# Kernel optimization log

Hardware: AMD Instinct MI355X
Metric: run time of the kernel (lower is better)

Reference implementation:

```python
import jax, jax.numpy as jnp
import numpy as np
import math

NUM_HEADS = 16
EPS = 1e-5

# Single-step spikingjelly LIFNode(tau=2.0, v_threshold=1.0, v_reset=0.0):
#   v = (x - 0)/tau = x/2 ; spike = heaviside(v - 1) = (x >= 2)
@jax.custom_vjp
def lif(x):
    return (x >= 2.0).astype(x.dtype)

def _lif_fwd(x):
    return (x >= 2.0).astype(x.dtype), x

def _lif_bwd(x, g):
    # sigmoid surrogate (alpha=4) on v - v_th, chained through dv/dx = 1/tau = 0.5
    s = jax.nn.sigmoid(4.0 * (0.5 * x - 1.0))
    return (g * (4.0 * s * (1.0 - s)) * 0.5,)

lif.defvjp(_lif_fwd, _lif_bwd)

def layernorm(x, gamma, beta):
    mu = jnp.mean(x, axis=-1, keepdims=True)
    var = jnp.var(x, axis=-1, keepdims=True)
    return (x - mu) * jax.lax.rsqrt(var + EPS) * gamma + beta

def mish(x):
    return x * jnp.tanh(jax.nn.softplus(x))

def setup_inputs() -> dict:
    key = jax.random.key(0)
    ks = jax.random.split(key, 8)
    B, Sq, Skv, dQ, dK, dV = 8, 1024, 1024, 1024, 1024, 1024
    def xavier_normal(k, shape):
        std = math.sqrt(2.0 / (shape[0] + shape[1]))
        return jax.random.normal(k, shape, jnp.float32) * std
    return {
        "Q": jax.random.normal(ks[0], (B, Sq, dQ), jnp.float32) * 2.0,
        "K": jax.random.normal(ks[1], (B, Skv, dK), jnp.float32) * 2.0,
        "adj_mask": (jax.random.uniform(ks[2], (B, 1, Sq, Skv)) < 0.7).astype(jnp.float32),
        "Wq": xavier_normal(ks[3], (dV, dQ)), "bq": jnp.zeros((dV,), jnp.float32),
        "Wk": xavier_normal(ks[4], (dV, dK)), "bk": jnp.zeros((dV,), jnp.float32),
        "Wv": xavier_normal(ks[5], (dV, dK)), "bv": jnp.zeros((dV,), jnp.float32),
        "Wo": xavier_normal(ks[6], (dV, dV)), "bo": jnp.zeros((dV,), jnp.float32),
        "g_q": jnp.ones((dV,), jnp.float32), "be_q": jnp.zeros((dV,), jnp.float32),
        "g_k": jnp.ones((dV,), jnp.float32), "be_k": jnp.zeros((dV,), jnp.float32),
    }

def reference(Q, K, adj_mask, Wq, bq, Wk, bk, Wv, bv, Wo, bo, g_q, be_q, g_k, be_k):
    B, Sq, _ = Q.shape
    Skv = K.shape[1]
    dV = Wq.shape[0]
    hd = dV // NUM_HEADS
    # LIF-gated projections (eval mode: dropout off)
    q = lif(layernorm(lif(Q) @ Wq.T + bq, g_q, be_q))          # [B,Sq,dV] binary
    v = lif(K) @ Wv.T + bv                                      # fc_v(k_lif(K))
    k = lif(layernorm(lif(K) @ Wk.T + bk, g_k, be_k))          # K(k_norm(fc_k(v_lif(K))))
    q = q.reshape(B, Sq, NUM_HEADS, hd).transpose(0, 2, 1, 3)  # [B,H,Sq,hd]
    k = k.reshape(B, Skv, NUM_HEADS, hd).transpose(0, 2, 1, 3)
    v = v.reshape(B, Skv, NUM_HEADS, hd).transpose(0, 2, 1, 3)
    scores = jnp.einsum('bhqd,bhkd->bhqk', q, k) / math.sqrt(hd)
    scores = scores * adj_mask                                  # multiplicative mask
    w = jax.nn.softmax(scores, axis=-1)
    out = jnp.einsum('bhqk,bhkd->bhqd', w, v)
    out = out.transpose(0, 2, 1, 3).reshape(B, Sq, dV)
    o = out @ Wo.T + bo
    return out + mish(o)
```

## Files before the change

kernel.cpp:

```cpp
#include <hip/hip_runtime.h>
#include <hip/hip_bf16.h>

typedef __attribute__((ext_vector_type(4))) float fx4;
typedef __attribute__((ext_vector_type(8))) short bv8;
typedef unsigned int u32;
typedef unsigned short u16;
typedef __hip_bfloat16 bf16;

#define DEVI static __device__ __forceinline__

static constexpr int NBATCH = 8;
static constexpr int SEQ = 1024;
static constexpr int DM  = 1024;
static constexpr int NH  = 16;
static constexpr int MROWS = NBATCH * SEQ;
static constexpr size_t SZ = (size_t)MROWS * DM;

DEVI void gl16(const void* g, void* l) {
  __builtin_amdgcn_global_load_lds((const __attribute__((address_space(1))) void*)g,
                                   (__attribute__((address_space(3))) void*)l, 16, 0, 0);
}
DEVI fx4 mfma_bf16(bv8 a, bv8 b, fx4 c) {
  return __builtin_amdgcn_mfma_f32_16x16x32_bf16(a, b, c, 0, 0, 0);
}

__global__ __launch_bounds__(256) void prep_weights(
    const float* __restrict__ wq, const float* __restrict__ wk,
    const float* __restrict__ wv, const float* __restrict__ wo,
    bf16* __restrict__ qh, bf16* __restrict__ qm, bf16* __restrict__ ql,
    bf16* __restrict__ kh, bf16* __restrict__ km, bf16* __restrict__ kl,
    bf16* __restrict__ vb, bf16* __restrict__ ob)
{
  int i = (blockIdx.x * 256 + threadIdx.x) * 4;
  int w = blockIdx.y;
  const float* src = (w == 0) ? wq : (w == 1) ? wk : (w == 2) ? wv : wo;
  fx4 v = *(const fx4*)&src[i];
  if (w < 2) {
    bf16* hi = (w == 0) ? qh : kh;
    bf16* mi = (w == 0) ? qm : km;
    bf16* lo = (w == 0) ? ql : kl;
#pragma unroll
    for (int j = 0; j < 4; j++) {
      float x = v[j];
      bf16 h = __float2bfloat16(x);
      float r1 = x - __bfloat162float(h);
      bf16 m = __float2bfloat16(r1);
      float r2 = r1 - __bfloat162float(m);
      hi[i + j] = h;
      mi[i + j] = m;
      lo[i + j] = __float2bfloat16(r2);
    }
  } else {
    bf16* dst = (w == 2) ? vb : ob;
#pragma unroll
    for (int j = 0; j < 4; j++) dst[i + j] = __float2bfloat16(v[j]);
  }
}

__global__ __launch_bounds__(256) void spike_kernel(const float* __restrict__ x, u16* __restrict__ o)
{
  size_t i = ((size_t)blockIdx.x * 256 + threadIdx.x) * 4;
  fx4 v = *(const fx4*)&x[i];
  u32 a = (v[0] >= 2.f ? 0x3F80u : 0u) | ((v[1] >= 2.f ? 0x3F80u : 0u) << 16);
  u32 b = (v[2] >= 2.f ? 0x3F80u : 0u) | ((v[3] >= 2.f ? 0x3F80u : 0u) << 16);
  u32* p = (u32*)(o + i);
  p[0] = a; p[1] = b;
}

__global__ __launch_bounds__(256) void maskpack_kernel(const float* __restrict__ m, u32* __restrict__ w)
{
  size_t gid = (size_t)blockIdx.x * 256 + threadIdx.x;
  unsigned long long bal = __ballot(m[gid] != 0.0f);
  int lane = threadIdx.x & 63;
  if (lane == 0) w[gid >> 5] = (u32)bal;
  else if (lane == 32) w[gid >> 5] = (u32)(bal >> 32);
}

template<int NB, int EPI>
__global__ __launch_bounds__(256) void gemm_bt(
    const bf16* __restrict__ A, const bf16* __restrict__ B0, const bf16* __restrict__ B1,
    const bf16* __restrict__ B2,
    const float* __restrict__ bias, const float* __restrict__ addsrc,
    float* __restrict__ Cf, bf16* __restrict__ Cb, int K, int N)
{
  __shared__ __attribute__((aligned(16))) bf16 sA[128 * 64];
  __shared__ __attribute__((aligned(16))) bf16 sB[NB * 128 * 64];
  const bf16* Bp[3] = {B0, B1, B2};
  const int tid = threadIdx.x;
  const int lane = tid & 63, wave = tid >> 6;
  const int wr = wave >> 1, wc = wave & 1;
  const int l15 = lane & 15, l4 = lane >> 4;
  const int rowBase = blockIdx.x * 128;
  const int colBase = blockIdx.y * 128;

  fx4 acc[4][4];
#pragma unroll
  for (int m = 0; m < 4; m++) {
#pragma unroll
    for (int n = 0; n < 4; n++) acc[m][n] = fx4{0.f, 0.f, 0.f, 0.f};
  }

  for (int kt = 0; kt < K; kt += 64) {
#pragma unroll
    for (int i = 0; i < 4; i++) {
      int c = i * 256 + tid;
      int r = c >> 3, cb = (c & 7) * 8;
      gl16(A + (size_t)(rowBase + r) * K + kt + cb, &sA[c * 8]);
    }
#pragma unroll
    for (int b = 0; b < NB; b++) {
#pragma unroll
      for (int i = 0; i < 4; i++) {
        int c = i * 256 + tid;
        int r = c >> 3, cb = (c & 7) * 8;
        gl16(Bp[b] + (size_t)(colBase + r) * K + kt + cb, &sB[b * 128 * 64 + c * 8]);
      }
    }
    __syncthreads();
#pragma unroll
    for (int kk = 0; kk < 2; kk++) {
      bv8 af[4];
#pragma unroll
      for (int m = 0; m < 4; m++)
        af[m] = *(const bv8*)&sA[(wr * 64 + m * 16 + l15) * 64 + kk * 32 + l4 * 8];
#pragma unroll
      for (int b = 0; b < NB; b++) {
#pragma unroll
        for (int n = 0; n < 4; n++) {
          bv8 bfr = *(const bv8*)&sB[b * 128 * 64 + (wc * 64 + n * 16 + l15) * 64 + kk * 32 + l4 * 8];
#pragma unroll
          for (int m = 0; m < 4; m++) acc[m][n] = mfma_bf16(af[m], bfr, acc[m][n]);
        }
      }
    }
    __syncthreads();
  }
#pragma unroll
  for (int n = 0; n < 4; n++) {
    int col = colBase + wc * 64 + n * 16 + l15;
    float bvv = bias[col];
#pragma unroll
    for (int m = 0; m < 4; m++) {
      int row0 = rowBase + wr * 64 + m * 16 + l4 * 4;
#pragma unroll
      for (int r = 0; r < 4; r++) {
        size_t idx = (size_t)(row0 + r) * N + col;
        float val = acc[m][n][r] + bvv;
        if (EPI == 0) {
          Cf[idx] = val;
        } else if (EPI == 1) {
          Cb[idx] = __float2bfloat16(val);
        } else {
          float sp = log1pf(__expf(val));
          Cf[idx] = addsrc[idx] + val * tanhf(sp);
        }
      }
    }
  }
}

__global__ __launch_bounds__(256) void lnlif_kernel(
    const float* __restrict__ x, const float* __restrict__ g, const float* __restrict__ be,
    u16* __restrict__ out)
{
  __shared__ float red[4];
  const int row = blockIdx.x;
  const int tid = threadIdx.x;
  fx4 v = *(const fx4*)&x[(size_t)row * DM + tid * 4];
  float s = v[0] + v[1] + v[2] + v[3];
#pragma unroll
  for (int off = 1; off < 64; off <<= 1) s += __shfl_xor(s, off, 64);
  if ((tid & 63) == 0) red[tid >> 6] = s;
  __syncthreads();
  float mean = (red[0] + red[1] + red[2] + red[3]) * (1.0f / 1024.0f);
  __syncthreads();
  float d0 = v[0] - mean, d1 = v[1] - mean, d2 = v[2] - mean, d3 = v[3] - mean;
  float ss = d0 * d0 + d1 * d1 + d2 * d2 + d3 * d3;
#pragma unroll
  for (int off = 1; off < 64; off <<= 1) ss += __shfl_xor(ss, off, 64);
  if ((tid & 63) == 0) red[tid >> 6] = ss;
  __syncthreads();
  float var = (red[0] + red[1] + red[2] + red[3]) * (1.0f / 1024.0f);
  float rstd = rsqrtf(var + 1e-5f);
  const int c = tid * 4;
  fx4 gg = *(const fx4*)&g[c];
  fx4 bb = *(const fx4*)&be[c];
  float y0 = d0 * rstd * gg[0] + bb[0];
  float y1 = d1 * rstd * gg[1] + bb[1];
  float y2 = d2 * rstd * gg[2] + bb[2];
  float y3 = d3 * rstd * gg[3] + bb[3];
  u32 a = (y0 >= 2.f ? 0x3F80u : 0u) | ((y1 >= 2.f ? 0x3F80u : 0u) << 16);
  u32 b = (y2 >= 2.f ? 0x3F80u : 0u) | ((y3 >= 2.f ? 0x3F80u : 0u) << 16);
  u32* p = (u32*)(out + (size_t)row * DM + c);
  p[0] = a; p[1] = b;
}

__global__ __launch_bounds__(256) void transpose_v(const bf16* __restrict__ v, bf16* __restrict__ vt)
{
  __shared__ bf16 t[64][72];
  const int tc = blockIdx.x, tr = blockIdx.y, b = blockIdx.z;
  const int tid = threadIdx.x;
  const size_t base = (size_t)b * SEQ * DM;
#pragma unroll
  for (int i = 0; i < 2; i++) {
    int c = i * 256 + tid;
    int r = c >> 3, cg = (c & 7) * 8;
    bv8 val = *(const bv8*)&v[base + (size_t)(tr * 64 + r) * DM + tc * 64 + cg];
#pragma unroll
    for (int j = 0; j < 8; j++) t[r][cg + j] = ((const bf16*)&val)[j];
  }
  __syncthreads();
#pragma unroll
  for (int i = 0; i < 2; i++) {
    int c = i * 256 + tid;
    int r = c >> 3, cg = (c & 7) * 8;
    bf16 tmp[8];
#pragma unroll
    for (int j = 0; j < 8; j++) tmp[j] = t[cg + j][r];
    *(bv8*)&vt[base + (size_t)(tc * 64 + r) * SEQ + tr * 64 + cg] = *(const bv8*)tmp;
  }
}

__global__ __launch_bounds__(256) void attn_kernel(
    const bf16* __restrict__ qb, const bf16* __restrict__ kb, const bf16* __restrict__ vt,
    const u32* __restrict__ mw, float* __restrict__ of, bf16* __restrict__ ob)
{
  __shared__ __attribute__((aligned(16))) bf16 sQ[64 * 64];
  __shared__ __attribute__((aligned(16))) bf16 sK[64 * 64];
  __shared__ __attribute__((aligned(16))) bf16 sV[64 * 64];
  __shared__ __attribute__((aligned(16))) bf16 sP[4][16 * 64];
  __shared__ u32 sM[128];
  const int qt = blockIdx.x, h = blockIdx.y, b = blockIdx.z;
  const int tid = threadIdx.x, lane = tid & 63, wave = tid >> 6;
  const int l15 = lane & 15, l4 = lane >> 4;
  const size_t qrow0 = (size_t)b * SEQ + qt * 64;

#pragma unroll
  for (int i = 0; i < 2; i++) {
    int c = i * 256 + tid;
    int r = c >> 3, cg = (c & 7) * 8;
    gl16(qb + (qrow0 + r) * DM + h * 64 + cg, &sQ[c * 8]);
  }
  __syncthreads();
  bv8 af[2];
  af[0] = *(const bv8*)&sQ[(wave * 16 + l15) * 64 + l4 * 8];
  af[1] = *(const bv8*)&sQ[(wave * 16 + l15) * 64 + 32 + l4 * 8];

  fx4 acc_o[4];
#pragma unroll
  for (int n = 0; n < 4; n++) acc_o[n] = fx4{0.f, 0.f, 0.f, 0.f};
  float rowsum[4] = {0.f, 0.f, 0.f, 0.f};

  for (int kvb = 0; kvb < SEQ; kvb += 64) {
#pragma unroll
    for (int i = 0; i < 2; i++) {
      int c = i * 256 + tid;
      int r = c >> 3, cg = (c & 7) * 8;
      gl16(kb + ((size_t)b * SEQ + kvb + r) * DM + h * 64 + cg, &sK[c * 8]);
      gl16(vt + (size_t)b * SEQ * DM + (size_t)(h * 64 + r) * SEQ + kvb + cg, &sV[c * 8]);
    }
    if (tid < 128) sM[tid] = mw[(qrow0 + (tid >> 1)) * 32 + (kvb >> 5) + (tid & 1)];
    __syncthreads();

    fx4 accs[4];
#pragma unroll
    for (int n = 0; n < 4; n++) accs[n] = fx4{0.f, 0.f, 0.f, 0.f};
#pragma unroll
    for (int kk = 0; kk < 2; kk++) {
#pragma unroll
      for (int n = 0; n < 4; n++) {
        bv8 bfk = *(const bv8*)&sK[(n * 16 + l15) * 64 + kk * 32 + l4 * 8];
        accs[n] = mfma_bf16(af[kk], bfk, accs[n]);
      }
    }
    float prow[4] = {0.f, 0.f, 0.f, 0.f};
#pragma unroll
    for (int n = 0; n < 4; n++) {
#pragma unroll
      for (int r = 0; r < 4; r++) {
        u32 wd = sM[((wave << 4) + (l4 << 2) + r) * 2 + (n >> 1)];
        float sc = accs[n][r] * 0.125f;
        float p = ((wd >> ((n & 1) * 16 + l15)) & 1u) ? __expf(sc) : 1.0f;
        prow[r] += p;
        sP[wave][((l4 << 2) + r) * 64 + n * 16 + l15] = __float2bfloat16(p);
      }
    }
#pragma unroll
    for (int r = 0; r < 4; r++) {
      float t2 = prow[r];
      t2 += __shfl_xor(t2, 1, 64);
      t2 += __shfl_xor(t2, 2, 64);
      t2 += __shfl_xor(t2, 4, 64);
      t2 += __shfl_xor(t2, 8, 64);
      rowsum[r] += t2;
    }
    __syncthreads();
#pragma unroll
    for (int kk = 0; kk < 2; kk++) {
      bv8 pa = *(const bv8*)&sP[wave][l15 * 64 + kk * 32 + l4 * 8];
#pragma unroll
      for (int n = 0; n < 4; n++) {
        bv8 bvv = *(const bv8*)&sV[(n * 16 + l15) * 64 + kk * 32 + l4 * 8];
        acc_o[n] = mfma_bf16(pa, bvv, acc_o[n]);
      }
    }
    __syncthreads();
  }
#pragma unroll
  for (int r = 0; r < 4; r++) {
    float inv = 1.0f / rowsum[r];
    size_t row = qrow0 + wave * 16 + (l4 << 2) + r;
#pragma unroll
    for (int n = 0; n < 4; n++) {
      size_t idx = row * DM + h * 64 + n * 16 + l15;
      float val = acc_o[n][r] * inv;
      of[idx] = val;
      ob[idx] = __float2bfloat16(val);
    }
  }
}

extern "C" void kernel_launch(void* const* d_in, const int* in_sizes, int n_in,
                              void* d_out, int out_size, void* d_ws, size_t ws_size,
                              hipStream_t stream) {
  (void)in_sizes; (void)n_in; (void)out_size; (void)ws_size;
  const float* Q    = (const float*)d_in[0];
  const float* Kin  = (const float*)d_in[1];
  const float* mask = (const float*)d_in[2];
  const float* Wq   = (const float*)d_in[3];
  const float* bq   = (const float*)d_in[4];
  const float* Wk   = (const float*)d_in[5];
  const float* bk   = (const float*)d_in[6];
  const float* Wv   = (const float*)d_in[7];
  const float* bv   = (const float*)d_in[8];
  const float* Wo   = (const float*)d_in[9];
  const float* bo   = (const float*)d_in[10];
  const float* g_q  = (const float*)d_in[11];
  const float* be_q = (const float*)d_in[12];
  const float* g_k  = (const float*)d_in[13];
  const float* be_k = (const float*)d_in[14];
  float* out = (float*)d_out;

  char* w = (char*)d_ws;
  size_t off = 0;
  auto alloc = [&](size_t bytes) -> char* {
    char* p = w + off;
    off += (bytes + 255) & ~(size_t)255;
    return p;
  };
  bf16* q_spike = (bf16*)alloc(SZ * 2);
  bf16* k_spike = (bf16*)alloc(SZ * 2);
  float* xq     = (float*)alloc(SZ * 4);
  float* xk     = (float*)alloc(SZ * 4);
  bf16* vb_     = (bf16*)alloc(SZ * 2);
  bf16* vtb     = (bf16*)alloc(SZ * 2);
  u32* mwords   = (u32*)alloc(SZ / 32 * 4);
  bf16* whq = (bf16*)alloc((size_t)DM * DM * 2);
  bf16* wmq = (bf16*)alloc((size_t)DM * DM * 2);
  bf16* wlq = (bf16*)alloc((size_t)DM * DM * 2);
  bf16* whk = (bf16*)alloc((size_t)DM * DM * 2);
  bf16* wmk = (bf16*)alloc((size_t)DM * DM * 2);
  bf16* wlk = (bf16*)alloc((size_t)DM * DM * 2);
  bf16* wvb = (bf16*)alloc((size_t)DM * DM * 2);
  bf16* wob = (bf16*)alloc((size_t)DM * DM * 2);
  bf16* qbn = q_spike;
  bf16* kbn = k_spike;
  float* attn_out = xq;
  bf16* attn_outb = (bf16*)xk;

  prep_weights<<<dim3(DM * DM / 1024, 4), 256, 0, stream>>>(Wq, Wk, Wv, Wo,
                                                            whq, wmq, wlq, whk, wmk, wlk, wvb, wob);
  spike_kernel<<<SZ / 1024, 256, 0, stream>>>(Q, (u16*)q_spike);
  spike_kernel<<<SZ / 1024, 256, 0, stream>>>(Kin, (u16*)k_spike);
  maskpack_kernel<<<SZ / 256, 256, 0, stream>>>(mask, mwords);

  gemm_bt<3, 0><<<dim3(64, 8), 256, 0, stream>>>(q_spike, whq, wmq, wlq, bq, nullptr, xq, nullptr, DM, DM);
  gemm_bt<3, 0><<<dim3(64, 8), 256, 0, stream>>>(k_spike, whk, wmk, wlk, bk, nullptr, xk, nullptr, DM, DM);
  gemm_bt<1, 1><<<dim3(64, 8), 256, 0, stream>>>(k_spike, wvb, nullptr, nullptr, bv, nullptr, nullptr, vb_, DM, DM);

  lnlif_kernel<<<MROWS, 256, 0, stream>>>(xq, g_q, be_q, (u16*)qbn);
  lnlif_kernel<<<MROWS, 256, 0, stream>>>(xk, g_k, be_k, (u16*)kbn);
  transpose_v<<<dim3(16, 16, NBATCH), 256, 0, stream>>>(vb_, vtb);

  attn_kernel<<<dim3(16, NH, NBATCH), 256, 0, stream>>>(qbn, kbn, vtb, mwords, attn_out, attn_outb);

  gemm_bt<1, 2><<<dim3(64, 8), 256, 0, stream>>>(attn_outb, wob, nullptr, nullptr, bo, attn_out, out, nullptr, DM, DM);
}
```

Baseline: 523.8 us.

## Double-buffer K/V tiles in attention with swizzled LDS and transposed mask words

The attention kernel now double-buffers the K, V and mask tiles so the next tile's global-to-LDS loads are issued while the current tile is computed, using one barrier per iteration instead of three. LDS layouts for K, V and P are XOR-swizzled to avoid bank conflicts. The packed mask is stored transposed so each block loads its mask words with vector loads. The row-sum shuffle reduction moves out of the loop, Q fragments are read directly from global memory, and exp becomes exp2 with a prescaled constant. It also adds s_setprio hints around the MFMA blocks. The cost is twice the LDS for K/V, and the single barrier relies on the per-wave sP buffer being safely reused across iterations.

```diff
diff --git a/kernel.cpp b/kernel.cpp
--- a/kernel.cpp
+++ b/kernel.cpp
@@ -72,8 +72,12 @@
   size_t gid = (size_t)blockIdx.x * 256 + threadIdx.x;
   unsigned long long bal = __ballot(m[gid] != 0.0f);
   int lane = threadIdx.x & 63;
-  if (lane == 0) w[gid >> 5] = (u32)bal;
-  else if (lane == 32) w[gid >> 5] = (u32)(bal >> 32);
+  u32 skv = (u32)(gid & 1023);
+  u32 sq  = (u32)((gid >> 10) & 1023);
+  u32 b   = (u32)(gid >> 20);
+  size_t oidx = (size_t)b * 32768 + (skv >> 5) * 1024 + sq;
+  if (lane == 0) w[oidx] = (u32)bal;
+  else if (lane == 32) w[oidx] = (u32)(bal >> 32);
 }
 
 template<int NB, int EPI>
@@ -223,92 +227,115 @@
 
 __global__ __launch_bounds__(256) void attn_kernel(
     const bf16* __restrict__ qb, const bf16* __restrict__ kb, const bf16* __restrict__ vt,
-    const u32* __restrict__ mw, float* __restrict__ of, bf16* __restrict__ ob)
-{
-  __shared__ __attribute__((aligned(16))) bf16 sQ[64 * 64];
-  __shared__ __attribute__((aligned(16))) bf16 sK[64 * 64];
-  __shared__ __attribute__((aligned(16))) bf16 sV[64 * 64];
+    const u32* __restrict__ mwT, float* __restrict__ of, bf16* __restrict__ ob)
+{
+  __shared__ __attribute__((aligned(16))) bf16 sK[2][64 * 64];
+  __shared__ __attribute__((aligned(16))) bf16 sV[2][64 * 64];
   __shared__ __attribute__((aligned(16))) bf16 sP[4][16 * 64];
-  __shared__ u32 sM[128];
+  __shared__ __attribute__((aligned(16))) u32 sM[2][128];
   const int qt = blockIdx.x, h = blockIdx.y, b = blockIdx.z;
   const int tid = threadIdx.x, lane = tid & 63, wave = tid >> 6;
   const int l15 = lane & 15, l4 = lane >> 4;
   const size_t qrow0 = (size_t)b * SEQ + qt * 64;
-
-#pragma unroll
-  for (int i = 0; i < 2; i++) {
-    int c = i * 256 + tid;
-    int r = c >> 3, cg = (c & 7) * 8;
-    gl16(qb + (qrow0 + r) * DM + h * 64 + cg, &sQ[c * 8]);
-  }
-  __syncthreads();
-  bv8 af[2];
-  af[0] = *(const bv8*)&sQ[(wave * 16 + l15) * 64 + l4 * 8];
-  af[1] = *(const bv8*)&sQ[(wave * 16 + l15) * 64 + 32 + l4 * 8];
-
-  fx4 acc_o[4];
-#pragma unroll
-  for (int n = 0; n < 4; n++) acc_o[n] = fx4{0.f, 0.f, 0.f, 0.f};
-  float rowsum[4] = {0.f, 0.f, 0.f, 0.f};
-
-  for (int kvb = 0; kvb < SEQ; kvb += 64) {
+  const bf16* kB = kb + (size_t)b * SEQ * DM + h * 64;
+  const bf16* vB = vt + (size_t)b * SEQ * DM + (size_t)(h * 64) * SEQ;
+  const u32*  mB = mwT + (size_t)b * 32768 + qt * 64;
+
+  auto STAGE = [&](int t, int buf) {
+    const int kvb = t * 64;
 #pragma unroll
     for (int i = 0; i < 2; i++) {
       int c = i * 256 + tid;
-      int r = c >> 3, cg = (c & 7) * 8;
-      gl16(kb + ((size_t)b * SEQ + kvb + r) * DM + h * 64 + cg, &sK[c * 8]);
-      gl16(vt + (size_t)b * SEQ * DM + (size_t)(h * 64 + r) * SEQ + kvb + cg, &sV[c * 8]);
-    }
-    if (tid < 128) sM[tid] = mw[(qrow0 + (tid >> 1)) * 32 + (kvb >> 5) + (tid & 1)];
-    __syncthreads();
+      int row = c >> 3;
+      int sb = ((c & 7) * 16) ^ ((row & 7) << 4);
+      gl16(kB + (size_t)(kvb + row) * DM + (sb >> 1), &sK[buf][c * 8]);
+      gl16(vB + (size_t)row * SEQ + kvb + (sb >> 1), &sV[buf][c * 8]);
+    }
+    if (tid < 32) {
+      int w = tid >> 4, rg = (tid & 15) * 4;
+      uint4 mv = *(const uint4*)&mB[(size_t)(t * 2 + w) * 1024 + rg];
+      *(uint4*)&sM[buf][w * 64 + rg] = mv;
+    }
+  };
+
+  bv8 af[2];
+#pragma unroll
+  for (int kk = 0; kk < 2; kk++)
+    af[kk] = *(const bv8*)&qb[(qrow0 + wave * 16 + l15) * DM + h * 64 + kk * 32 + l4 * 8];
+
+  fx4 acc_o[4];
+#pragma unroll
+  for (int n = 0; n < 4; n++) acc_o[n] = fx4{0.f, 0.f, 0.f, 0.f};
+  float psum[4] = {0.f, 0.f, 0.f, 0.f};
+
+  char* sPw = (char*)sP[wave];
+  STAGE(0, 0);
+
+  for (int t = 0; t < 16; t++) {
+    const int cur = t & 1;
+    asm volatile("s_waitcnt vmcnt(0) lgkmcnt(0)" ::: "memory");
+    __builtin_amdgcn_s_barrier();
+    if (t < 15) STAGE(t + 1, cur ^ 1);
+
+    const char* sKc = (const char*)sK[cur];
+    const char* sVc = (const char*)sV[cur];
 
     fx4 accs[4];
 #pragma unroll
     for (int n = 0; n < 4; n++) accs[n] = fx4{0.f, 0.f, 0.f, 0.f};
+    __builtin_amdgcn_s_setprio(1);
 #pragma unroll
     for (int kk = 0; kk < 2; kk++) {
 #pragma unroll
       for (int n = 0; n < 4; n++) {
-        bv8 bfk = *(const bv8*)&sK[(n * 16 + l15) * 64 + kk * 32 + l4 * 8];
-        accs[n] = mfma_bf16(af[kk], bfk, accs[n]);
-      }
-    }
-    float prow[4] = {0.f, 0.f, 0.f, 0.f};
+        int row = n * 16 + l15;
+        bv8 bk8 = *(const bv8*)(sKc + row * 128 + ((kk * 64 + l4 * 16) ^ ((row & 7) << 4)));
+        accs[n] = mfma_bf16(af[kk], bk8, accs[n]);
+      }
+    }
+    __builtin_amdgcn_s_setprio(0);
+
+    uint4 m0 = *(const uint4*)&sM[cur][wave * 16 + l4 * 4];
+    uint4 m1 = *(const uint4*)&sM[cur][64 + wave * 16 + l4 * 4];
+    u32 sh0[4] = {m0.x >> l15, m0.y >> l15, m0.z >> l15, m0.w >> l15};
+    u32 sh1[4] = {m1.x >> l15, m1.y >> l15, m1.z >> l15, m1.w >> l15};
+
 #pragma unroll
     for (int n = 0; n < 4; n++) {
 #pragma unroll
       for (int r = 0; r < 4; r++) {
-        u32 wd = sM[((wave << 4) + (l4 << 2) + r) * 2 + (n >> 1)];
-        float sc = accs[n][r] * 0.125f;
-        float p = ((wd >> ((n & 1) * 16 + l15)) & 1u) ? __expf(sc) : 1.0f;
-        prow[r] += p;
-        sP[wave][((l4 << 2) + r) * 64 + n * 16 + l15] = __float2bfloat16(p);
-      }
-    }
-#pragma unroll
-    for (int r = 0; r < 4; r++) {
-      float t2 = prow[r];
-      t2 += __shfl_xor(t2, 1, 64);
-      t2 += __shfl_xor(t2, 2, 64);
-      t2 += __shfl_xor(t2, 4, 64);
-      t2 += __shfl_xor(t2, 8, 64);
-      rowsum[r] += t2;
-    }
-    __syncthreads();
+        float e = exp2f(accs[n][r] * 0.18033688011112042f);
+        u32 s = (n < 2) ? sh0[r] : sh1[r];
+        float p = ((s >> ((n & 1) * 16)) & 1u) ? e : 1.0f;
+        psum[r] += p;
+        int pr = l4 * 4 + r;
+        int cb = (n * 16 + l15) * 2;
+        *(bf16*)(sPw + pr * 128 + (cb ^ ((pr & 7) << 4))) = __float2bfloat16(p);
+      }
+    }
+
+    __builtin_amdgcn_s_setprio(1);
 #pragma unroll
     for (int kk = 0; kk < 2; kk++) {
-      bv8 pa = *(const bv8*)&sP[wave][l15 * 64 + kk * 32 + l4 * 8];
+      bv8 pa = *(const bv8*)(sPw + l15 * 128 + ((kk * 64 + l4 * 16) ^ ((l15 & 7) << 4)));
 #pragma unroll
       for (int n = 0; n < 4; n++) {
-        bv8 bvv = *(const bv8*)&sV[(n * 16 + l15) * 64 + kk * 32 + l4 * 8];
-        acc_o[n] = mfma_bf16(pa, bvv, acc_o[n]);
-      }
-    }
-    __syncthreads();
-  }
+        int row = n * 16 + l15;
+        bv8 bv8v = *(const bv8*)(sVc + row * 128 + ((kk * 64 + l4 * 16) ^ ((row & 7) << 4)));
+        acc_o[n] = mfma_bf16(pa, bv8v, acc_o[n]);
+      }
+    }
+    __builtin_amdgcn_s_setprio(0);
+  }
+
 #pragma unroll
   for (int r = 0; r < 4; r++) {
-    float inv = 1.0f / rowsum[r];
+    float t2 = psum[r];
+    t2 += __shfl_xor(t2, 1, 64);
+    t2 += __shfl_xor(t2, 2, 64);
+    t2 += __shfl_xor(t2, 4, 64);
+    t2 += __shfl_xor(t2, 8, 64);
+    float inv = 1.0f / t2;
     size_t row = qrow0 + wave * 16 + (l4 << 2) + r;
 #pragma unroll
     for (int n = 0; n < 4; n++) {
```

Result: faster. 495.1 us (-5.5%).
